# Kernel tuning notes

Hardware: AMD Instinct MI355X
Metric: run time of the kernel (lower is better)

Reference implementation:

```python
import jax, jax.numpy as jnp
import numpy as np

B, N, D = 32, 256, 3
NF, L = 16, 3


def _fully_connected(n):
    # Same ordering as connect_fully: for i in range(n) for j in range(n) if i != j
    a = np.repeat(np.arange(n), n)
    b = np.tile(np.arange(n), n)
    m = a != b
    return a[m].astype(np.int32), b[m].astype(np.int32)


def setup_inputs() -> dict:
    key = jax.random.key(0)
    ks = jax.random.split(key, 12)
    src, dst = _fully_connected(N)
    s = 0.1  # small param scale for numerical stability
    return {
        "xs": jax.random.normal(ks[0], (B, N, D), jnp.float32),
        "vs": jax.random.normal(ks[1], (B, N, D), jnp.float32),
        "charges": jax.random.normal(ks[2], (B * N, 1), jnp.float32),
        "W_in": s * jax.random.normal(ks[3], (1, NF), jnp.float32),
        "b_in": jnp.zeros((NF,), jnp.float32),
        "W_v": s * jax.random.normal(ks[4], (L, NF, 1), jnp.float32),
        "We1": s * jax.random.normal(ks[5], (L, 2 * NF + 1, NF), jnp.float32),
        "be1": jnp.zeros((L, NF), jnp.float32),
        "We2": s * jax.random.normal(ks[6], (L, NF, NF), jnp.float32),
        "be2": jnp.zeros((L, NF), jnp.float32),
        "Wx": s * jax.random.normal(ks[7], (L, NF, 1), jnp.float32),
        "Wh1": s * jax.random.normal(ks[8], (L, 2 * NF, NF), jnp.float32),
        "bh1": jnp.zeros((L, NF), jnp.float32),
        "src": jnp.asarray(src),
        "dst": jnp.asarray(dst),
    }


def reference(xs, vs, charges, W_in, b_in, W_v, We1, be1, We2, be2, Wx, Wh1, bh1, src, dst):
    b, n, d = xs.shape
    # node scalar features from charges (ndata['f'])
    h = jax.nn.relu(charges.reshape(b, n, 1) @ W_in + b_in)  # [B,N,nf]
    x = xs
    n_layers = We1.shape[0]
    for l in range(n_layers):
        # fully-connected edge gather + subtract (edata['d'])
        de = x[:, dst] - x[:, src]                         # [B,E,3]
        r2 = jnp.sum(de * de, axis=-1, keepdims=True)      # [B,E,1]
        e_in = jnp.concatenate([h[:, src], h[:, dst], r2], axis=-1)  # [B,E,2nf+1]
        m = jax.nn.relu(e_in @ We1[l] + be1[l])
        m = jax.nn.relu(m @ We2[l] + be2[l])               # [B,E,nf]
        w = m @ Wx[l]                                      # [B,E,1]
        # equivariant coordinate update: scatter-add edge vectors into dst nodes
        agg_x = jnp.zeros_like(x).at[:, dst].add(de * w) / (n - 1)
        x = x + agg_x + vs * (h @ W_v[l])                  # velocity term (ndata['vel'])
        m_agg = jnp.zeros_like(h).at[:, dst].add(m)        # [B,N,nf]
        h = h + jax.nn.relu(jnp.concatenate([h, m_agg], axis=-1) @ Wh1[l] + bh1[l])
    # OurDynamics returns (se3_out['1'] + xs).view(-1, n_dimension)
    return x.reshape(-1, d)
```

## Files before the change

kernel.cpp:

```cpp
#include <hip/hip_runtime.h>

#define NN 256
#define NF 16

typedef _Float16 half4 __attribute__((ext_vector_type(4)));
typedef float f32x4 __attribute__((ext_vector_type(4)));

#define XA_OFF 0
#define XB_OFF 32768
#define HA_OFF 65536
#define HB_OFF 196608
#define SUA_OFF 327680
#define SVA_OFF 458752
#define SUB_OFF 589824
#define SVB_OFF 720896

__global__ __launch_bounds__(256)
void layer0_kernel(const float* __restrict__ xs, const float* __restrict__ vs,
                   const float* __restrict__ charges,
                   const float* __restrict__ W_in, const float* __restrict__ b_in,
                   const float* __restrict__ W_v, const float* __restrict__ We1_l,
                   const float* __restrict__ be1_l, const float* __restrict__ We2_l,
                   const float* __restrict__ be2_l, const float* __restrict__ Wx_l,
                   const float* __restrict__ Wh1_l, const float* __restrict__ bh1_l,
                   const float* __restrict__ We1_n, const float* __restrict__ be1_n,
                   float* __restrict__ x_out, float* __restrict__ h_out,
                   float* __restrict__ su_out, float* __restrict__ sv_out) {
    __shared__ __align__(16) float sSU[NN * NF];
    __shared__ __align__(16) float sX[NN * 4];
    __shared__ __align__(16) float sHg[64 * NF];
    __shared__ float sWs[256], sWd[256];
    __shared__ __align__(16) float sSV8[8][NF];
    __shared__ __align__(16) float sH8[8][NF + 1];
    __shared__ float sWh1s[512];
    __shared__ float sWa[256], sWb[256];
    __shared__ float sbe1n[NF];
    __shared__ float sh_new[8][NF + 1];
    __shared__ float sg[8][NF];

    const int tid  = threadIdx.x;
    const int b    = blockIdx.x >> 5;
    const int oct  = blockIdx.x & 31;
    const int n0l  = 8 * oct;
    const size_t n0 = (size_t)b * NN + n0l;
    const int w    = tid >> 6;
    const int lane = tid & 63;
    const int c    = lane & 15;
    const int g    = lane >> 4;

    sWs[tid] = We1_l[tid];
    sWd[tid] = We1_l[256 + tid];
    sWh1s[tid]       = Wh1_l[tid];
    sWh1s[256 + tid] = Wh1_l[256 + tid];
    {
        const int f = tid >> 4, kk = tid & 15;
        sWa[kk * NF + f] = We1_n[tid];
        sWb[kk * NF + f] = We1_n[256 + tid];
        if (tid < NF) sbe1n[tid] = be1_n[tid];
    }
    {
        const size_t base = ((size_t)b * NN + tid) * 3;
        sX[tid * 4 + 0] = xs[base + 0];
        sX[tid * 4 + 1] = xs[base + 1];
        sX[tid * 4 + 2] = xs[base + 2];
        sX[tid * 4 + 3] = 0.f;
    }

    const int nl = tid >> 4, k = tid & 15;
    const float win  = W_in[k];
    const float bin  = b_in[k];
    const float be1k = be1_l[k];
    const int i0 = n0l >> 6;
    const int r0 = (n0l & 63) >> 4;
    const int halfsel = (n0l >> 3) & 1;
    const int own = ((nl >> 3) == halfsel);
#pragma unroll
    for (int i = 0; i < 4; ++i) {
#pragma unroll
        for (int r = 0; r < 4; ++r) {
            const float cq = charges[(size_t)b * NN + 64 * i + 16 * r + nl];
            const float hf = fmaxf(fmaf(cq, win, bin), 0.f);
            sHg[(16 * r + nl) * NF + k] = hf;
            if (i == i0 && r == r0 && own) sH8[nl & 7][k] = hf;
        }
        __syncthreads();
#pragma unroll
        for (int r = 0; r < 4; ++r) {
            const float4* hn = (const float4*)&sHg[(16 * r + nl) * NF];
            const float4 h0q = hn[0], h1q = hn[1], h2q = hn[2], h3q = hn[3];
            float u = 0.f;
#pragma unroll
            for (int q = 0; q < 4; ++q) {
                const float4 hq = (q == 0) ? h0q : (q == 1) ? h1q : (q == 2) ? h2q : h3q;
                u = fmaf(hq.x, sWs[(4 * q + 0) * NF + k], u);
                u = fmaf(hq.y, sWs[(4 * q + 1) * NF + k], u);
                u = fmaf(hq.z, sWs[(4 * q + 2) * NF + k], u);
                u = fmaf(hq.w, sWs[(4 * q + 3) * NF + k], u);
            }
            sSU[(64 * i + 16 * r + nl) * NF + k] = u;
            if (i == i0 && r == r0 && own) {
                float v = be1k;
#pragma unroll
                for (int q = 0; q < 4; ++q) {
                    const float4 hq = (q == 0) ? h0q : (q == 1) ? h1q : (q == 2) ? h2q : h3q;
                    v = fmaf(hq.x, sWd[(4 * q + 0) * NF + k], v);
                    v = fmaf(hq.y, sWd[(4 * q + 1) * NF + k], v);
                    v = fmaf(hq.z, sWd[(4 * q + 2) * NF + k], v);
                    v = fmaf(hq.w, sWd[(4 * q + 3) * NF + k], v);
                }
                sSV8[nl & 7][k] = v;
            }
        }
        __syncthreads();
    }

    const int j0 = n0l + w, j1 = n0l + 4 + w;
    const float4 xj0 = *(const float4*)&sX[4 * j0];
    const float4 xj1 = *(const float4*)&sX[4 * j1];
    half4 afrag;
    afrag.x = (_Float16)We2_l[(4 * g + 0) * NF + c];
    afrag.y = (_Float16)We2_l[(4 * g + 1) * NF + c];
    afrag.z = (_Float16)We2_l[(4 * g + 2) * NF + c];
    afrag.w = (_Float16)We2_l[(4 * g + 3) * NF + c];
    const float4 v40 = *(const float4*)&sSV8[w][4 * g];
    const float4 v41 = *(const float4*)&sSV8[4 + w][4 * g];
    const float4 wr4  = *(const float4*)(We1_l + 512 + 4 * g);
    const float4 be2f = *(const float4*)(be2_l + 4 * g);
    const float4 wxf  = *(const float4*)(Wx_l + 4 * g);
    f32x4 cb;
    cb.x = be2f.x; cb.y = be2f.y; cb.z = be2f.z; cb.w = be2f.w;

    float Sw0 = 0.f, Swx0 = 0.f, Swy0 = 0.f, Swz0 = 0.f;
    float Sw1 = 0.f, Swx1 = 0.f, Swy1 = 0.f, Swz1 = 0.f;
    float g00 = 0.f, g01 = 0.f, g02 = 0.f, g03 = 0.f;
    float g10 = 0.f, g11 = 0.f, g12 = 0.f, g13 = 0.f;

    const float* su_l = &sSU[c * NF + 4 * g];
    const float* x_l  = &sX[4 * c];

#pragma unroll 2
    for (int t = 0; t < 16; ++t) {
        const float4 u4  = *(const float4*)(su_l + 256 * t);
        const float4 xs4 = *(const float4*)(x_l + 64 * t);
        const int s = 16 * t + c;
        {
            const float dx = xj0.x - xs4.x, dy = xj0.y - xs4.y, dz = xj0.z - xs4.z;
            const float r2 = fmaf(dx, dx, fmaf(dy, dy, dz * dz));
            const float m0 = fmaxf(fmaf(r2, wr4.x, u4.x + v40.x), 0.f);
            const float m1 = fmaxf(fmaf(r2, wr4.y, u4.y + v40.y), 0.f);
            const float m2 = fmaxf(fmaf(r2, wr4.z, u4.z + v40.z), 0.f);
            const float m3 = fmaxf(fmaf(r2, wr4.w, u4.w + v40.w), 0.f);
            half4 bfrag;
            bfrag.x = (_Float16)m0; bfrag.y = (_Float16)m1;
            bfrag.z = (_Float16)m2; bfrag.w = (_Float16)m3;
            const f32x4 acc = __builtin_amdgcn_mfma_f32_16x16x16f16(afrag, bfrag, cb, 0, 0, 0);
            const float e0 = fmaxf(acc.x, 0.f);
            const float e1 = fmaxf(acc.y, 0.f);
            const float e2 = fmaxf(acc.z, 0.f);
            const float e3 = fmaxf(acc.w, 0.f);
            float wp = e0 * wxf.x;
            wp = fmaf(e1, wxf.y, wp);
            wp = fmaf(e2, wxf.z, wp);
            wp = fmaf(e3, wxf.w, wp);
            const float gsel = (s != j0) ? 1.f : 0.f;
            g00 = fmaf(e0, gsel, g00);
            g01 = fmaf(e1, gsel, g01);
            g02 = fmaf(e2, gsel, g02);
            g03 = fmaf(e3, gsel, g03);
            Sw0 += wp;
            Swx0 = fmaf(wp, xs4.x, Swx0);
            Swy0 = fmaf(wp, xs4.y, Swy0);
            Swz0 = fmaf(wp, xs4.z, Swz0);
        }
        {
            const float dx = xj1.x - xs4.x, dy = xj1.y - xs4.y, dz = xj1.z - xs4.z;
            const float r2 = fmaf(dx, dx, fmaf(dy, dy, dz * dz));
            const float m0 = fmaxf(fmaf(r2, wr4.x, u4.x + v41.x), 0.f);
            const float m1 = fmaxf(fmaf(r2, wr4.y, u4.y + v41.y), 0.f);
            const float m2 = fmaxf(fmaf(r2, wr4.z, u4.z + v41.z), 0.f);
            const float m3 = fmaxf(fmaf(r2, wr4.w, u4.w + v41.w), 0.f);
            half4 bfrag;
            bfrag.x = (_Float16)m0; bfrag.y = (_Float16)m1;
            bfrag.z = (_Float16)m2; bfrag.w = (_Float16)m3;
            const f32x4 acc = __builtin_amdgcn_mfma_f32_16x16x16f16(afrag, bfrag, cb, 0, 0, 0);
            const float e0 = fmaxf(acc.x, 0.f);
            const float e1 = fmaxf(acc.y, 0.f);
            const float e2 = fmaxf(acc.z, 0.f);
            const float e3 = fmaxf(acc.w, 0.f);
            float wp = e0 * wxf.x;
            wp = fmaf(e1, wxf.y, wp);
            wp = fmaf(e2, wxf.z, wp);
            wp = fmaf(e3, wxf.w, wp);
            const float gsel = (s != j1) ? 1.f : 0.f;
            g10 = fmaf(e0, gsel, g10);
            g11 = fmaf(e1, gsel, g11);
            g12 = fmaf(e2, gsel, g12);
            g13 = fmaf(e3, gsel, g13);
            Sw1 += wp;
            Swx1 = fmaf(wp, xs4.x, Swx1);
            Swy1 = fmaf(wp, xs4.y, Swy1);
            Swz1 = fmaf(wp, xs4.z, Swz1);
        }
    }

#pragma unroll
    for (int off = 1; off < 64; off <<= 1) {
        Sw0  += __shfl_xor(Sw0,  off, 64);  Sw1  += __shfl_xor(Sw1,  off, 64);
        Swx0 += __shfl_xor(Swx0, off, 64);  Swx1 += __shfl_xor(Swx1, off, 64);
        Swy0 += __shfl_xor(Swy0, off, 64);  Swy1 += __shfl_xor(Swy1, off, 64);
        Swz0 += __shfl_xor(Swz0, off, 64);  Swz1 += __shfl_xor(Swz1, off, 64);
    }
#pragma unroll
    for (int off = 1; off < 16; off <<= 1) {
        g00 += __shfl_xor(g00, off, 64);  g10 += __shfl_xor(g10, off, 64);
        g01 += __shfl_xor(g01, off, 64);  g11 += __shfl_xor(g11, off, 64);
        g02 += __shfl_xor(g02, off, 64);  g12 += __shfl_xor(g12, off, 64);
        g03 += __shfl_xor(g03, off, 64);  g13 += __shfl_xor(g13, off, 64);
    }
    if ((lane & 15) == 0) {
        *(float4*)&sg[w][4 * g]     = make_float4(g00, g01, g02, g03);
        *(float4*)&sg[w + 4][4 * g] = make_float4(g10, g11, g12, g13);
    }
    __syncthreads();

    const int is0 = (lane < 16);
    const int is1 = (lane >= 32 && lane < 48);
    if (is0 || is1) {
        const int f = lane & 15;
        const int slot = is0 ? w : (w + 4);
        const int jm   = is0 ? j0 : j1;
        const float SwS = is0 ? Sw0  : Sw1;
        const float SxS = is0 ? Swx0 : Swx1;
        const float SyS = is0 ? Swy0 : Swy1;
        const float SzS = is0 ? Swz0 : Swz1;
        const float4 xjm = is0 ? xj0 : xj1;
        const size_t nj = (size_t)b * NN + jm;
        float hd = bh1_l[f];
        float hv = 0.f;
#pragma unroll
        for (int kk = 0; kk < NF; ++kk) {
            const float hjk = sH8[slot][kk];
            hd = fmaf(hjk, sWh1s[kk * NF + f], hd);
            hv = fmaf(hjk, W_v[kk], hv);
        }
#pragma unroll
        for (int kk = 0; kk < NF; ++kk) {
            hd = fmaf(sg[slot][kk], sWh1s[(NF + kk) * NF + f], hd);
        }
        const float hnew = sH8[slot][f] + fmaxf(hd, 0.f);
        sh_new[slot][f] = hnew;
        h_out[nj * NF + f] = hnew;
        if (f < 3) {
            const float xc = (f == 0) ? xjm.x : ((f == 1) ? xjm.y : xjm.z);
            const float Sc = (f == 0) ? SxS  : ((f == 1) ? SyS  : SzS);
            const float agg = (SwS * xc - Sc) * (1.f / 255.f);
            const float xnew = xc + agg + vs[nj * 3 + f] * hv;
            x_out[nj * 4 + f] = xnew;
        }
        if (f == 3) x_out[nj * 4 + 3] = 0.f;
    }

    __syncthreads();
    if (tid < 128) {
        const int jd = tid >> 4, kk = tid & 15;
        float u = 0.f, v = sbe1n[kk];
#pragma unroll
        for (int f = 0; f < NF; ++f) {
            const float hf = sh_new[jd][f];
            u = fmaf(hf, sWa[kk * NF + f], u);
            v = fmaf(hf, sWb[kk * NF + f], v);
        }
        su_out[(n0 + jd) * NF + kk] = u;
        sv_out[(n0 + jd) * NF + kk] = v;
    }
}

__global__ __launch_bounds__(256)
void layer_kernel(const float* __restrict__ x_in, const float* __restrict__ h_in,
                  const float* __restrict__ su_in, const float* __restrict__ sv_in,
                  float* __restrict__ x_out, float* __restrict__ h_out,
                  float* __restrict__ su_out, float* __restrict__ sv_out,
                  const float* __restrict__ vs, const float* __restrict__ Wv_l,
                  const float* __restrict__ We1_l, const float* __restrict__ We2_l,
                  const float* __restrict__ be2_l, const float* __restrict__ Wx_l,
                  const float* __restrict__ Wh1_l, const float* __restrict__ bh1_l,
                  const float* __restrict__ We1_n, const float* __restrict__ be1_n,
                  int final_layer) {
    __shared__ __align__(16) float sSU[NN * NF];
    __shared__ __align__(16) float sX[NN * 4];
    __shared__ float sWh1s[512];
    __shared__ float sWa[256];
    __shared__ float sWb[256];
    __shared__ float sbe1n[NF];
    __shared__ float sh_new[8][NF + 1];
    __shared__ float sg[8][NF];

    const int tid  = threadIdx.x;
    const int b    = blockIdx.x >> 5;
    const int oct  = blockIdx.x & 31;
    const int n0l  = 8 * oct;
    const size_t n0 = (size_t)b * NN + n0l;
    const int w    = tid >> 6;
    const int lane = tid & 63;
    const int c    = lane & 15;
    const int g    = lane >> 4;

    sWh1s[tid]       = Wh1_l[tid];
    sWh1s[256 + tid] = Wh1_l[256 + tid];
    if (!final_layer) {
        const int f = tid >> 4, k = tid & 15;
        sWa[k * NF + f] = We1_n[tid];
        sWb[k * NF + f] = We1_n[256 + tid];
        if (tid < NF) sbe1n[tid] = be1_n[tid];
    }
    {
        const float4* gsu = (const float4*)(su_in + (size_t)b * NN * NF);
        float4* lsu = (float4*)sSU;
        lsu[tid]        = gsu[tid];
        lsu[256 + tid]  = gsu[256 + tid];
        lsu[512 + tid]  = gsu[512 + tid];
        lsu[768 + tid]  = gsu[768 + tid];
        const float4* gx = (const float4*)(x_in + (size_t)b * NN * 4);
        ((float4*)sX)[tid] = gx[tid];
    }
    __syncthreads();

    const int j0 = n0l + w, j1 = n0l + 4 + w;
    const float4 xj0 = *(const float4*)&sX[4 * j0];
    const float4 xj1 = *(const float4*)&sX[4 * j1];
    half4 afrag;
    afrag.x = (_Float16)We2_l[(4 * g + 0) * NF + c];
    afrag.y = (_Float16)We2_l[(4 * g + 1) * NF + c];
    afrag.z = (_Float16)We2_l[(4 * g + 2) * NF + c];
    afrag.w = (_Float16)We2_l[(4 * g + 3) * NF + c];
    const float4 v40  = *(const float4*)(sv_in + ((size_t)b * NN + j0) * NF + 4 * g);
    const float4 v41  = *(const float4*)(sv_in + ((size_t)b * NN + j1) * NF + 4 * g);
    const float4 wr4  = *(const float4*)(We1_l + 512 + 4 * g);
    const float4 be2f = *(const float4*)(be2_l + 4 * g);
    const float4 wxf  = *(const float4*)(Wx_l + 4 * g);
    f32x4 cb;
    cb.x = be2f.x; cb.y = be2f.y; cb.z = be2f.z; cb.w = be2f.w;

    float Sw0 = 0.f, Swx0 = 0.f, Swy0 = 0.f, Swz0 = 0.f;
    float Sw1 = 0.f, Swx1 = 0.f, Swy1 = 0.f, Swz1 = 0.f;
    float g00 = 0.f, g01 = 0.f, g02 = 0.f, g03 = 0.f;
    float g10 = 0.f, g11 = 0.f, g12 = 0.f, g13 = 0.f;

    const float* su_l = &sSU[c * NF + 4 * g];
    const float* x_l  = &sX[4 * c];

#pragma unroll 2
    for (int t = 0; t < 16; ++t) {
        const float4 u4  = *(const float4*)(su_l + 256 * t);
        const float4 xs4 = *(const float4*)(x_l + 64 * t);
        const int s = 16 * t + c;
        {
            const float dx = xj0.x - xs4.x, dy = xj0.y - xs4.y, dz = xj0.z - xs4.z;
            const float r2 = fmaf(dx, dx, fmaf(dy, dy, dz * dz));
            const float m0 = fmaxf(fmaf(r2, wr4.x, u4.x + v40.x), 0.f);
            const float m1 = fmaxf(fmaf(r2, wr4.y, u4.y + v40.y), 0.f);
            const float m2 = fmaxf(fmaf(r2, wr4.z, u4.z + v40.z), 0.f);
            const float m3 = fmaxf(fmaf(r2, wr4.w, u4.w + v40.w), 0.f);
            half4 bfrag;
            bfrag.x = (_Float16)m0; bfrag.y = (_Float16)m1;
            bfrag.z = (_Float16)m2; bfrag.w = (_Float16)m3;
            const f32x4 acc = __builtin_amdgcn_mfma_f32_16x16x16f16(afrag, bfrag, cb, 0, 0, 0);
            const float e0 = fmaxf(acc.x, 0.f);
            const float e1 = fmaxf(acc.y, 0.f);
            const float e2 = fmaxf(acc.z, 0.f);
            const float e3 = fmaxf(acc.w, 0.f);
            float wp = e0 * wxf.x;
            wp = fmaf(e1, wxf.y, wp);
            wp = fmaf(e2, wxf.z, wp);
            wp = fmaf(e3, wxf.w, wp);
            const float gsel = (s != j0) ? 1.f : 0.f;
            g00 = fmaf(e0, gsel, g00);
            g01 = fmaf(e1, gsel, g01);
            g02 = fmaf(e2, gsel, g02);
            g03 = fmaf(e3, gsel, g03);
            Sw0 += wp;
            Swx0 = fmaf(wp, xs4.x, Swx0);
            Swy0 = fmaf(wp, xs4.y, Swy0);
            Swz0 = fmaf(wp, xs4.z, Swz0);
        }
        {
            const float dx = xj1.x - xs4.x, dy = xj1.y - xs4.y, dz = xj1.z - xs4.z;
            const float r2 = fmaf(dx, dx, fmaf(dy, dy, dz * dz));
            const float m0 = fmaxf(fmaf(r2, wr4.x, u4.x + v41.x), 0.f);
            const float m1 = fmaxf(fmaf(r2, wr4.y, u4.y + v41.y), 0.f);
            const float m2 = fmaxf(fmaf(r2, wr4.z, u4.z + v41.z), 0.f);
            const float m3 = fmaxf(fmaf(r2, wr4.w, u4.w + v41.w), 0.f);
            half4 bfrag;
            bfrag.x = (_Float16)m0; bfrag.y = (_Float16)m1;
            bfrag.z = (_Float16)m2; bfrag.w = (_Float16)m3;
            const f32x4 acc = __builtin_amdgcn_mfma_f32_16x16x16f16(afrag, bfrag, cb, 0, 0, 0);
            const float e0 = fmaxf(acc.x, 0.f);
            const float e1 = fmaxf(acc.y, 0.f);
            const float e2 = fmaxf(acc.z, 0.f);
            const float e3 = fmaxf(acc.w, 0.f);
            float wp = e0 * wxf.x;
            wp = fmaf(e1, wxf.y, wp);
            wp = fmaf(e2, wxf.z, wp);
            wp = fmaf(e3, wxf.w, wp);
            const float gsel = (s != j1) ? 1.f : 0.f;
            g10 = fmaf(e0, gsel, g10);
            g11 = fmaf(e1, gsel, g11);
            g12 = fmaf(e2, gsel, g12);
            g13 = fmaf(e3, gsel, g13);
            Sw1 += wp;
            Swx1 = fmaf(wp, xs4.x, Swx1);
            Swy1 = fmaf(wp, xs4.y, Swy1);
            Swz1 = fmaf(wp, xs4.z, Swz1);
        }
    }

#pragma unroll
    for (int off = 1; off < 64; off <<= 1) {
        Sw0  += __shfl_xor(Sw0,  off, 64);  Sw1  += __shfl_xor(Sw1,  off, 64);
        Swx0 += __shfl_xor(Swx0, off, 64);  Swx1 += __shfl_xor(Swx1, off, 64);
        Swy0 += __shfl_xor(Swy0, off, 64);  Swy1 += __shfl_xor(Swy1, off, 64);
        Swz0 += __shfl_xor(Swz0, off, 64);  Swz1 += __shfl_xor(Swz1, off, 64);
    }
#pragma unroll
    for (int off = 1; off < 16; off <<= 1) {
        g00 += __shfl_xor(g00, off, 64);  g10 += __shfl_xor(g10, off, 64);
        g01 += __shfl_xor(g01, off, 64);  g11 += __shfl_xor(g11, off, 64);
        g02 += __shfl_xor(g02, off, 64);  g12 += __shfl_xor(g12, off, 64);
        g03 += __shfl_xor(g03, off, 64);  g13 += __shfl_xor(g13, off, 64);
    }
    if ((lane & 15) == 0) {
        *(float4*)&sg[w][4 * g]     = make_float4(g00, g01, g02, g03);
        *(float4*)&sg[w + 4][4 * g] = make_float4(g10, g11, g12, g13);
    }
    __syncthreads();

    const int is0 = (lane < 16);
    const int is1 = (lane >= 32 && lane < 48);
    if (is0 || is1) {
        const int f = lane & 15;
        const int slot = is0 ? w : (w + 4);
        const int jm   = is0 ? j0 : j1;
        const float SwS = is0 ? Sw0  : Sw1;
        const float SxS = is0 ? Swx0 : Swx1;
        const float SyS = is0 ? Swy0 : Swy1;
        const float SzS = is0 ? Swz0 : Swz1;
        const float4 xjm = is0 ? xj0 : xj1;
        const size_t nj = (size_t)b * NN + jm;
        float hd = bh1_l[f];
        float hv = 0.f;
#pragma unroll
        for (int k = 0; k < NF; ++k) {
            const float hjk = h_in[nj * NF + k];
            hd = fmaf(hjk, sWh1s[k * NF + f], hd);
            hv = fmaf(hjk, Wv_l[k], hv);
        }
#pragma unroll
        for (int k = 0; k < NF; ++k) {
            hd = fmaf(sg[slot][k], sWh1s[(NF + k) * NF + f], hd);
        }
        const float hnew = h_in[nj * NF + f] + fmaxf(hd, 0.f);
        sh_new[slot][f] = hnew;
        if (!final_layer) h_out[nj * NF + f] = hnew;
        if (f < 3) {
            const float xc = (f == 0) ? xjm.x : ((f == 1) ? xjm.y : xjm.z);
            const float Sc = (f == 0) ? SxS  : ((f == 1) ? SyS  : SzS);
            const float agg = (SwS * xc - Sc) * (1.f / 255.f);
            const float xnew = xc + agg + vs[nj * 3 + f] * hv;
            if (final_layer) x_out[nj * 3 + f] = xnew;
            else             x_out[nj * 4 + f] = xnew;
        }
        if (!final_layer && f == 3) x_out[nj * 4 + 3] = 0.f;
    }

    if (!final_layer) {
        __syncthreads();
        if (tid < 128) {
            const int jd = tid >> 4, k = tid & 15;
            float u = 0.f, v = sbe1n[k];
#pragma unroll
            for (int f = 0; f < NF; ++f) {
                const float hf = sh_new[jd][f];
                u = fmaf(hf, sWa[k * NF + f], u);
                v = fmaf(hf, sWb[k * NF + f], v);
            }
            su_out[(n0 + jd) * NF + k] = u;
            sv_out[(n0 + jd) * NF + k] = v;
        }
    }
}

extern "C" void kernel_launch(void* const* d_in, const int* in_sizes, int n_in,
                              void* d_out, int out_size, void* d_ws, size_t ws_size,
                              hipStream_t stream) {
    const float* xs      = (const float*)d_in[0];
    const float* vs      = (const float*)d_in[1];
    const float* charges = (const float*)d_in[2];
    const float* W_in    = (const float*)d_in[3];
    const float* b_in    = (const float*)d_in[4];
    const float* W_v     = (const float*)d_in[5];
    const float* We1     = (const float*)d_in[6];
    const float* be1     = (const float*)d_in[7];
    const float* We2     = (const float*)d_in[8];
    const float* be2     = (const float*)d_in[9];
    const float* Wx      = (const float*)d_in[10];
    const float* Wh1     = (const float*)d_in[11];
    const float* bh1     = (const float*)d_in[12];

    float* ws = (float*)d_ws;
    float* xA  = ws + XA_OFF;
    float* xB  = ws + XB_OFF;
    float* hA  = ws + HA_OFF;
    float* hB  = ws + HB_OFF;
    float* suA = ws + SUA_OFF;
    float* svA = ws + SVA_OFF;
    float* suB = ws + SUB_OFF;
    float* svB = ws + SVB_OFF;
    float* out = (float*)d_out;

    hipLaunchKernelGGL(layer0_kernel, dim3(1024), dim3(256), 0, stream,
                       xs, vs, charges, W_in, b_in,
                       W_v + 0 * 16, We1 + 0 * 528, be1 + 0 * 16, We2 + 0 * 256,
                       be2 + 0 * 16, Wx + 0 * 16, Wh1 + 0 * 512, bh1 + 0 * 16,
                       We1 + 1 * 528, be1 + 1 * 16,
                       xA, hA, suA, svA);
    hipLaunchKernelGGL(layer_kernel, dim3(1024), dim3(256), 0, stream,
                       xA, hA, suA, svA, xB, hB, suB, svB,
                       vs, W_v + 1 * 16, We1 + 1 * 528, We2 + 1 * 256,
                       be2 + 1 * 16, Wx + 1 * 16, Wh1 + 1 * 512, bh1 + 1 * 16,
                       We1 + 2 * 528, be1 + 2 * 16, 0);
    hipLaunchKernelGGL(layer_kernel, dim3(1024), dim3(256), 0, stream,
                       xB, hB, suB, svB, out, hA, suA, svA,
                       vs, W_v + 2 * 16, We1 + 2 * 528, We2 + 2 * 256,
                       be2 + 2 * 16, Wx + 2 * 16, Wh1 + 2 * 512, bh1 + 2 * 16,
                       We1 + 2 * 528, be1 + 2 * 16, 1);
}
```

Measured before the change: 131.8 us.

## Halve nodes per block and read source features from global instead of LDS

The layer kernel now handles 4 destination nodes per block instead of 8, doubling the grid to 2048 blocks. It drops the 16 KB shared-memory staging of the su table and reads it directly from global or L2 inside the edge loop, and it adds a min-blocks-per-CU launch bound. The aim is to cut LDS footprint and register pressure so more blocks are resident and the per-block staging cost goes away. In exchange each block reloads su from global, the per-block setup is amortised over half as many nodes, and each edge loop now issues one MFMA chain per wave instead of two.

```diff
diff --git a/kernel.cpp b/kernel.cpp
--- a/kernel.cpp
+++ b/kernel.cpp
@@ -275,7 +275,7 @@
     }
 }
 
-__global__ __launch_bounds__(256)
+__global__ __launch_bounds__(256, 8)
 void layer_kernel(const float* __restrict__ x_in, const float* __restrict__ h_in,
                   const float* __restrict__ su_in, const float* __restrict__ sv_in,
                   float* __restrict__ x_out, float* __restrict__ h_out,
@@ -286,19 +286,17 @@
                   const float* __restrict__ Wh1_l, const float* __restrict__ bh1_l,
                   const float* __restrict__ We1_n, const float* __restrict__ be1_n,
                   int final_layer) {
-    __shared__ __align__(16) float sSU[NN * NF];
     __shared__ __align__(16) float sX[NN * 4];
     __shared__ float sWh1s[512];
     __shared__ float sWa[256];
     __shared__ float sWb[256];
     __shared__ float sbe1n[NF];
-    __shared__ float sh_new[8][NF + 1];
-    __shared__ float sg[8][NF];
+    __shared__ __align__(16) float sh_new[4][NF + 1];
+    __shared__ __align__(16) float sg[4][NF];
 
     const int tid  = threadIdx.x;
-    const int b    = blockIdx.x >> 5;
-    const int oct  = blockIdx.x & 31;
-    const int n0l  = 8 * oct;
+    const int b    = blockIdx.x >> 6;
+    const int n0l  = (blockIdx.x & 63) * 4;
     const size_t n0 = (size_t)b * NN + n0l;
     const int w    = tid >> 6;
     const int lane = tid & 63;
@@ -314,138 +312,87 @@
         if (tid < NF) sbe1n[tid] = be1_n[tid];
     }
     {
-        const float4* gsu = (const float4*)(su_in + (size_t)b * NN * NF);
-        float4* lsu = (float4*)sSU;
-        lsu[tid]        = gsu[tid];
-        lsu[256 + tid]  = gsu[256 + tid];
-        lsu[512 + tid]  = gsu[512 + tid];
-        lsu[768 + tid]  = gsu[768 + tid];
         const float4* gx = (const float4*)(x_in + (size_t)b * NN * 4);
         ((float4*)sX)[tid] = gx[tid];
     }
     __syncthreads();
 
-    const int j0 = n0l + w, j1 = n0l + 4 + w;
-    const float4 xj0 = *(const float4*)&sX[4 * j0];
-    const float4 xj1 = *(const float4*)&sX[4 * j1];
+    const int j = n0l + w;
+    const float4 xj = *(const float4*)&sX[4 * j];
     half4 afrag;
     afrag.x = (_Float16)We2_l[(4 * g + 0) * NF + c];
     afrag.y = (_Float16)We2_l[(4 * g + 1) * NF + c];
     afrag.z = (_Float16)We2_l[(4 * g + 2) * NF + c];
     afrag.w = (_Float16)We2_l[(4 * g + 3) * NF + c];
-    const float4 v40  = *(const float4*)(sv_in + ((size_t)b * NN + j0) * NF + 4 * g);
-    const float4 v41  = *(const float4*)(sv_in + ((size_t)b * NN + j1) * NF + 4 * g);
+    const float4 v4   = *(const float4*)(sv_in + ((size_t)b * NN + j) * NF + 4 * g);
     const float4 wr4  = *(const float4*)(We1_l + 512 + 4 * g);
+    const float4 wxf  = *(const float4*)(Wx_l + 4 * g);
     const float4 be2f = *(const float4*)(be2_l + 4 * g);
-    const float4 wxf  = *(const float4*)(Wx_l + 4 * g);
     f32x4 cb;
     cb.x = be2f.x; cb.y = be2f.y; cb.z = be2f.z; cb.w = be2f.w;
 
-    float Sw0 = 0.f, Swx0 = 0.f, Swy0 = 0.f, Swz0 = 0.f;
-    float Sw1 = 0.f, Swx1 = 0.f, Swy1 = 0.f, Swz1 = 0.f;
-    float g00 = 0.f, g01 = 0.f, g02 = 0.f, g03 = 0.f;
-    float g10 = 0.f, g11 = 0.f, g12 = 0.f, g13 = 0.f;
-
-    const float* su_l = &sSU[c * NF + 4 * g];
+    float Sw = 0.f, Swx = 0.f, Swy = 0.f, Swz = 0.f;
+    float g0 = 0.f, g1 = 0.f, g2 = 0.f, g3 = 0.f;
+
+    const float* su_p = su_in + (size_t)b * NN * NF + c * NF + 4 * g;
     const float* x_l  = &sX[4 * c];
 
 #pragma unroll 2
     for (int t = 0; t < 16; ++t) {
-        const float4 u4  = *(const float4*)(su_l + 256 * t);
+        const float4 u4  = *(const float4*)(su_p + 256 * t);
         const float4 xs4 = *(const float4*)(x_l + 64 * t);
         const int s = 16 * t + c;
-        {
-            const float dx = xj0.x - xs4.x, dy = xj0.y - xs4.y, dz = xj0.z - xs4.z;
-            const float r2 = fmaf(dx, dx, fmaf(dy, dy, dz * dz));
-            const float m0 = fmaxf(fmaf(r2, wr4.x, u4.x + v40.x), 0.f);
-            const float m1 = fmaxf(fmaf(r2, wr4.y, u4.y + v40.y), 0.f);
-            const float m2 = fmaxf(fmaf(r2, wr4.z, u4.z + v40.z), 0.f);
-            const float m3 = fmaxf(fmaf(r2, wr4.w, u4.w + v40.w), 0.f);
-            half4 bfrag;
-            bfrag.x = (_Float16)m0; bfrag.y = (_Float16)m1;
-            bfrag.z = (_Float16)m2; bfrag.w = (_Float16)m3;
-            const f32x4 acc = __builtin_amdgcn_mfma_f32_16x16x16f16(afrag, bfrag, cb, 0, 0, 0);
-            const float e0 = fmaxf(acc.x, 0.f);
-            const float e1 = fmaxf(acc.y, 0.f);
-            const float e2 = fmaxf(acc.z, 0.f);
-            const float e3 = fmaxf(acc.w, 0.f);
-            float wp = e0 * wxf.x;
-            wp = fmaf(e1, wxf.y, wp);
-            wp = fmaf(e2, wxf.z, wp);
-            wp = fmaf(e3, wxf.w, wp);
-            const float gsel = (s != j0) ? 1.f : 0.f;
-            g00 = fmaf(e0, gsel, g00);
-            g01 = fmaf(e1, gsel, g01);
-            g02 = fmaf(e2, gsel, g02);
-            g03 = fmaf(e3, gsel, g03);
-            Sw0 += wp;
-            Swx0 = fmaf(wp, xs4.x, Swx0);
-            Swy0 = fmaf(wp, xs4.y, Swy0);
-            Swz0 = fmaf(wp, xs4.z, Swz0);
-        }
-        {
-            const float dx = xj1.x - xs4.x, dy = xj1.y - xs4.y, dz = xj1.z - xs4.z;
-            const float r2 = fmaf(dx, dx, fmaf(dy, dy, dz * dz));
-            const float m0 = fmaxf(fmaf(r2, wr4.x, u4.x + v41.x), 0.f);
-            const float m1 = fmaxf(fmaf(r2, wr4.y, u4.y + v41.y), 0.f);
-            const float m2 = fmaxf(fmaf(r2, wr4.z, u4.z + v41.z), 0.f);
-            const float m3 = fmaxf(fmaf(r2, wr4.w, u4.w + v41.w), 0.f);
-            half4 bfrag;
-            bfrag.x = (_Float16)m0; bfrag.y = (_Float16)m1;
-            bfrag.z = (_Float16)m2; bfrag.w = (_Float16)m3;
-            const f32x4 acc = __builtin_amdgcn_mfma_f32_16x16x16f16(afrag, bfrag, cb, 0, 0, 0);
-            const float e0 = fmaxf(acc.x, 0.f);
-            const float e1 = fmaxf(acc.y, 0.f);
-            const float e2 = fmaxf(acc.z, 0.f);
-            const float e3 = fmaxf(acc.w, 0.f);
-            float wp = e0 * wxf.x;
-            wp = fmaf(e1, wxf.y, wp);
-            wp = fmaf(e2, wxf.z, wp);
-            wp = fmaf(e3, wxf.w, wp);
-            const float gsel = (s != j1) ? 1.f : 0.f;
-            g10 = fmaf(e0, gsel, g10);
-            g11 = fmaf(e1, gsel, g11);
-            g12 = fmaf(e2, gsel, g12);
-            g13 = fmaf(e3, gsel, g13);
-            Sw1 += wp;
-            Swx1 = fmaf(wp, xs4.x, Swx1);
-            Swy1 = fmaf(wp, xs4.y, Swy1);
-            Swz1 = fmaf(wp, xs4.z, Swz1);
-        }
+        const float dx = xj.x - xs4.x, dy = xj.y - xs4.y, dz = xj.z - xs4.z;
+        const float r2 = fmaf(dx, dx, fmaf(dy, dy, dz * dz));
+        const float m0 = fmaxf(fmaf(r2, wr4.x, u4.x + v4.x), 0.f);
+        const float m1 = fmaxf(fmaf(r2, wr4.y, u4.y + v4.y), 0.f);
+        const float m2 = fmaxf(fmaf(r2, wr4.z, u4.z + v4.z), 0.f);
+        const float m3 = fmaxf(fmaf(r2, wr4.w, u4.w + v4.w), 0.f);
+        half4 bfrag;
+        bfrag.x = (_Float16)m0; bfrag.y = (_Float16)m1;
+        bfrag.z = (_Float16)m2; bfrag.w = (_Float16)m3;
+        const f32x4 acc = __builtin_amdgcn_mfma_f32_16x16x16f16(afrag, bfrag, cb, 0, 0, 0);
+        const float e0 = fmaxf(acc.x, 0.f);
+        const float e1 = fmaxf(acc.y, 0.f);
+        const float e2 = fmaxf(acc.z, 0.f);
+        const float e3 = fmaxf(acc.w, 0.f);
+        float wp = e0 * wxf.x;
+        wp = fmaf(e1, wxf.y, wp);
+        wp = fmaf(e2, wxf.z, wp);
+        wp = fmaf(e3, wxf.w, wp);
+        const float gsel = (s != j) ? 1.f : 0.f;
+        g0 = fmaf(e0, gsel, g0);
+        g1 = fmaf(e1, gsel, g1);
+        g2 = fmaf(e2, gsel, g2);
+        g3 = fmaf(e3, gsel, g3);
+        Sw += wp;
+        Swx = fmaf(wp, xs4.x, Swx);
+        Swy = fmaf(wp, xs4.y, Swy);
+        Swz = fmaf(wp, xs4.z, Swz);
     }
 
 #pragma unroll
     for (int off = 1; off < 64; off <<= 1) {
-        Sw0  += __shfl_xor(Sw0,  off, 64);  Sw1  += __shfl_xor(Sw1,  off, 64);
-        Swx0 += __shfl_xor(Swx0, off, 64);  Swx1 += __shfl_xor(Swx1, off, 64);
-        Swy0 += __shfl_xor(Swy0, off, 64);  Swy1 += __shfl_xor(Swy1, off, 64);
-        Swz0 += __shfl_xor(Swz0, off, 64);  Swz1 += __shfl_xor(Swz1, off, 64);
+        Sw  += __shfl_xor(Sw,  off, 64);
+        Swx += __shfl_xor(Swx, off, 64);
+        Swy += __shfl_xor(Swy, off, 64);
+        Swz += __shfl_xor(Swz, off, 64);
     }
 #pragma unroll
     for (int off = 1; off < 16; off <<= 1) {
-        g00 += __shfl_xor(g00, off, 64);  g10 += __shfl_xor(g10, off, 64);
-        g01 += __shfl_xor(g01, off, 64);  g11 += __shfl_xor(g11, off, 64);
-        g02 += __shfl_xor(g02, off, 64);  g12 += __shfl_xor(g12, off, 64);
-        g03 += __shfl_xor(g03, off, 64);  g13 += __shfl_xor(g13, off, 64);
+        g0 += __shfl_xor(g0, off, 64);
+        g1 += __shfl_xor(g1, off, 64);
+        g2 += __shfl_xor(g2, off, 64);
+        g3 += __shfl_xor(g3, off, 64);
     }
     if ((lane & 15) == 0) {
-        *(float4*)&sg[w][4 * g]     = make_float4(g00, g01, g02, g03);
-        *(float4*)&sg[w + 4][4 * g] = make_float4(g10, g11, g12, g13);
+        *(float4*)&sg[w][4 * g] = make_float4(g0, g1, g2, g3);
     }
     __syncthreads();
 
-    const int is0 = (lane < 16);
-    const int is1 = (lane >= 32 && lane < 48);
-    if (is0 || is1) {
-        const int f = lane & 15;
-        const int slot = is0 ? w : (w + 4);
-        const int jm   = is0 ? j0 : j1;
-        const float SwS = is0 ? Sw0  : Sw1;
-        const float SxS = is0 ? Swx0 : Swx1;
-        const float SyS = is0 ? Swy0 : Swy1;
-        const float SzS = is0 ? Swz0 : Swz1;
-        const float4 xjm = is0 ? xj0 : xj1;
-        const size_t nj = (size_t)b * NN + jm;
+    if (lane < 16) {
+        const int f = lane;
+        const size_t nj = (size_t)b * NN + j;
         float hd = bh1_l[f];
         float hv = 0.f;
 #pragma unroll
@@ -456,15 +403,15 @@
         }
 #pragma unroll
         for (int k = 0; k < NF; ++k) {
-            hd = fmaf(sg[slot][k], sWh1s[(NF + k) * NF + f], hd);
+            hd = fmaf(sg[w][k], sWh1s[(NF + k) * NF + f], hd);
         }
         const float hnew = h_in[nj * NF + f] + fmaxf(hd, 0.f);
-        sh_new[slot][f] = hnew;
+        sh_new[w][f] = hnew;
         if (!final_layer) h_out[nj * NF + f] = hnew;
         if (f < 3) {
-            const float xc = (f == 0) ? xjm.x : ((f == 1) ? xjm.y : xjm.z);
-            const float Sc = (f == 0) ? SxS  : ((f == 1) ? SyS  : SzS);
-            const float agg = (SwS * xc - Sc) * (1.f / 255.f);
+            const float xc = (f == 0) ? xj.x : ((f == 1) ? xj.y : xj.z);
+            const float Sc = (f == 0) ? Swx : ((f == 1) ? Swy : Swz);
+            const float agg = (Sw * xc - Sc) * (1.f / 255.f);
             const float xnew = xc + agg + vs[nj * 3 + f] * hv;
             if (final_layer) x_out[nj * 3 + f] = xnew;
             else             x_out[nj * 4 + f] = xnew;
@@ -474,7 +421,7 @@
 
     if (!final_layer) {
         __syncthreads();
-        if (tid < 128) {
+        if (tid < 64) {
             const int jd = tid >> 4, k = tid & 15;
             float u = 0.f, v = sbe1n[k];
 #pragma unroll
@@ -523,12 +470,12 @@
                        be2 + 0 * 16, Wx + 0 * 16, Wh1 + 0 * 512, bh1 + 0 * 16,
                        We1 + 1 * 528, be1 + 1 * 16,
                        xA, hA, suA, svA);
-    hipLaunchKernelGGL(layer_kernel, dim3(1024), dim3(256), 0, stream,
+    hipLaunchKernelGGL(layer_kernel, dim3(2048), dim3(256), 0, stream,
                        xA, hA, suA, svA, xB, hB, suB, svB,
                        vs, W_v + 1 * 16, We1 + 1 * 528, We2 + 1 * 256,
                        be2 + 1 * 16, Wx + 1 * 16, Wh1 + 1 * 512, bh1 + 1 * 16,
                        We1 + 2 * 528, be1 + 2 * 16, 0);
-    hipLaunchKernelGGL(layer_kernel, dim3(1024), dim3(256), 0, stream,
+    hipLaunchKernelGGL(layer_kernel, dim3(2048), dim3(256), 0, stream,
                        xB, hB, suB, svB, out, hA, suA, svA,
                        vs, W_v + 2 * 16, We1 + 2 * 528, We2 + 2 * 256,
                        be2 + 2 * 16, Wx + 2 * 16, Wh1 + 2 * 512, bh1 + 2 * 16,
```

Result: slower. 135.3 us (+2.6%).
